# Optimization experiments

Measured on AMD Instinct MI355X. Metric: run time of the kernel, lower is better.

## Reference

```python
import jax, jax.numpy as jnp
import numpy as np

DIM = 128; MOTION = 128; HEADS = 8; WS = 8; B2 = 4; H = 192; W = 192; HID = 512

def _ln(x, w, b, eps=1e-5):
    m = x.mean(-1, keepdims=True)
    v = ((x - m) ** 2).mean(-1, keepdims=True)
    return (x - m) / jnp.sqrt(v + eps) * w + b

def _win_part(x, ws):
    B, Hh, Ww, C = x.shape
    x = x.reshape(B, Hh // ws, ws, Ww // ws, ws, C).transpose(0, 1, 3, 2, 4, 5)
    return x.reshape(-1, ws * ws, C)

def _win_rev(win, ws, Hh, Ww):
    nwB, N, C = win.shape
    B = nwB // ((Hh // ws) * (Ww // ws))
    x = win.reshape(B, Hh // ws, Ww // ws, ws, ws, C).transpose(0, 1, 3, 2, 4, 5)
    return x.reshape(B, Hh, Ww, C)

def setup_inputs() -> dict:
    key = jax.random.key(0)
    ks = jax.random.split(key, 12)
    def lin(k, o, i):
        return jax.random.normal(k, (o, i), jnp.float32) * 0.02
    return {
        "x": jax.random.normal(ks[0], (B2, H * W, DIM), jnp.float32),
        "cor": jax.random.uniform(ks[1], (B2, H * W, 2), dtype=jnp.float32),
        "q_w": lin(ks[2], DIM, DIM),
        "kv_w": lin(ks[3], 2 * DIM, DIM),
        "cor_w": lin(ks[4], MOTION, 2),
        "proj_w": lin(ks[5], DIM, DIM), "proj_b": jnp.zeros((DIM,), jnp.float32),
        "mproj_w": lin(ks[6], MOTION, MOTION), "mproj_b": jnp.zeros((MOTION,), jnp.float32),
        "norm1_w": jnp.ones((DIM,), jnp.float32), "norm1_b": jnp.zeros((DIM,), jnp.float32),
        "norm2_w": jnp.ones((DIM,), jnp.float32), "norm2_b": jnp.zeros((DIM,), jnp.float32),
        "fc1_w": lin(ks[7], HID, DIM), "fc1_b": jnp.zeros((HID,), jnp.float32),
        "dw_w": jax.random.normal(ks[8], (HID, 1, 3, 3), jnp.float32) * 0.1,
        "dw_b": jnp.zeros((HID,), jnp.float32),
        "fc2_w": lin(ks[9], DIM, HID), "fc2_b": jnp.zeros((DIM,), jnp.float32),
    }

def _attn(x1, x2, cor, q_w, kv_w, cor_w, proj_w, proj_b, mproj_w, mproj_b):
    # x1,x2: (nwB, N, C) windowed query / cross-frame key-value; cor: (nwB, N, 2)
    B, N, C = x1.shape
    hd = C // HEADS
    mh = MOTION // HEADS
    scale = hd ** -0.5
    q = (x1 @ q_w.T).reshape(B, N, HEADS, hd).transpose(0, 2, 1, 3)
    kv = (x2 @ kv_w.T).reshape(B, N, 2, HEADS, hd).transpose(2, 0, 3, 1, 4)
    k, v = kv[0], kv[1]
    ce = cor @ cor_w.T                                   # (B, N, MOTION)
    ceh = ce.reshape(B, N, HEADS, mh).transpose(0, 2, 1, 3)
    attn = jax.nn.softmax(jnp.einsum('bhnd,bhmd->bhnm', q, k) * scale, axis=-1)
    xo = jnp.einsum('bhnm,bhmd->bhnd', attn, v).transpose(0, 2, 1, 3).reshape(B, N, C)
    crev = jnp.einsum('bhnm,bhmd->bhnd', attn, ceh).transpose(0, 2, 1, 3).reshape(B, N, MOTION)
    motion = (crev - ce) @ mproj_w.T + mproj_b
    return xo @ proj_w.T + proj_b, motion

def _mlp(x, fc1_w, fc1_b, dw_w, dw_b, fc2_w, fc2_b):
    B, N, _ = x.shape
    h = x @ fc1_w.T + fc1_b                              # (B, N, HID)
    hm = h.transpose(0, 2, 1).reshape(B, HID, H, W)
    hm = jax.lax.conv_general_dilated(hm, dw_w, (1, 1), 'SAME',
                                      feature_group_count=HID,
                                      dimension_numbers=('NCHW', 'OIHW', 'NCHW'))
    hm = hm + dw_b[None, :, None, None]
    h = jax.nn.gelu(hm.reshape(B, HID, N).transpose(0, 2, 1), approximate=False)
    return h @ fc2_w.T + fc2_b

def reference(x, cor, q_w, kv_w, cor_w, proj_w, proj_b, mproj_w, mproj_b,
              norm1_w, norm1_b, norm2_w, norm2_b, fc1_w, fc1_b, dw_w, dw_b, fc2_w, fc2_b):
    shortcut = x
    xn = _ln(x, norm1_w, norm1_b).reshape(B2, H, W, DIM)
    cm = cor.reshape(B2, H, W, 2)
    xw = _win_part(xn, WS)                               # (nwB, 64, DIM)
    cw = _win_part(cm, WS)
    nwB = xw.shape[0]
    xr = jnp.concatenate([xw[nwB // 2:], xw[:nwB // 2]], axis=0)
    xa, xm = _attn(xw, xr, cw, q_w, kv_w, cor_w, proj_w, proj_b, mproj_w, mproj_b)
    xa = _win_rev(xa, WS, H, W).reshape(B2, H * W, DIM)
    xm = _win_rev(xm, WS, H, W).reshape(B2, H * W, MOTION)
    x = shortcut + xa
    x = x + _mlp(_ln(x, norm2_w, norm2_b), fc1_w, fc1_b, dw_w, dw_b, fc2_w, fc2_b)
    return x, xm
```

## Files before the change

kernel.cpp:

```cpp
#include <hip/hip_runtime.h>
#include <hip/hip_bf16.h>
#include <math.h>

#define NB 4
#define IMG 192
#define HW (IMG*IMG)
#define T_TOT (NB*HW)
#define HID 512
#define NWB 2304
#define WPB 576
#define NWS 24

typedef __bf16 bf16;
typedef __bf16 bf8 __attribute__((ext_vector_type(8)));
typedef __bf16 bf4 __attribute__((ext_vector_type(4)));
typedef float f32x4 __attribute__((ext_vector_type(4)));

#define MFMA(a,b,c) __builtin_amdgcn_mfma_f32_16x16x32_bf16(a,b,c,0,0,0)

__device__ __forceinline__ int swz128(int row, int col){ return row*128 + (col ^ ((row&7)<<3)); }

__device__ __forceinline__ bf8 zero_bf8(){
  bf8 z = { (bf16)0.f,(bf16)0.f,(bf16)0.f,(bf16)0.f,(bf16)0.f,(bf16)0.f,(bf16)0.f,(bf16)0.f };
  return z;
}
__device__ __forceinline__ f32x4 zero_f4(){ f32x4 z = {0.f,0.f,0.f,0.f}; return z; }

__global__ void k_cvt(const float* __restrict__ s, bf16* __restrict__ d, int n, float scale){
  int i = blockIdx.x*256 + threadIdx.x;
  if (i < n) d[i] = (bf16)(s[i]*scale);
}

__global__ void k_a2(const float* __restrict__ mproj_w, const float* __restrict__ cor_w,
                     bf16* __restrict__ a2w){
  int idx = blockIdx.x*256 + threadIdx.x;
  if (idx >= 4096) return;
  int o = idx >> 5, k = idx & 31;
  float acc = 0.f;
  if (k < 16){
    int h = k >> 1, c = k & 1;
    #pragma unroll
    for (int i=0;i<16;i++)
      acc += mproj_w[o*128 + h*16 + i] * cor_w[(h*16+i)*2 + c];
  }
  a2w[o*32 + k] = (bf16)acc;
}

__global__ __launch_bounds__(256) void k_ln1(
    const float* __restrict__ x, const float* __restrict__ cor,
    const float* __restrict__ n1w, const float* __restrict__ n1b,
    bf16* __restrict__ xn, bf16* __restrict__ cwb)
{
  int tid = threadIdx.x, wm = tid>>6, l = tid&63;
  int lr = l & 15, tg = l >> 4;
  int t = blockIdx.x*16 + wm*4 + tg;

  const float* xp = x + (size_t)t*128 + lr*8;
  float4 a = *(const float4*)xp;
  float4 b4 = *(const float4*)(xp+4);
  float s  = a.x+a.y+a.z+a.w + b4.x+b4.y+b4.z+b4.w;
  float sq = a.x*a.x+a.y*a.y+a.z*a.z+a.w*a.w + b4.x*b4.x+b4.y*b4.y+b4.z*b4.z+b4.w*b4.w;
  #pragma unroll
  for (int m=1;m<16;m<<=1){ s += __shfl_xor(s,m,16); sq += __shfl_xor(sq,m,16); }
  float mean = s * (1.0f/128.0f);
  float var  = sq * (1.0f/128.0f) - mean*mean;
  float rstd = rsqrtf(var + 1e-5f);

  float4 nw0 = *(const float4*)(n1w + lr*8), nw1 = *(const float4*)(n1w + lr*8 + 4);
  float4 nb0 = *(const float4*)(n1b + lr*8), nb1 = *(const float4*)(n1b + lr*8 + 4);

  bf8 o;
  o[0] = (bf16)((a.x -mean)*rstd*nw0.x + nb0.x);
  o[1] = (bf16)((a.y -mean)*rstd*nw0.y + nb0.y);
  o[2] = (bf16)((a.z -mean)*rstd*nw0.z + nb0.z);
  o[3] = (bf16)((a.w -mean)*rstd*nw0.w + nb0.w);
  o[4] = (bf16)((b4.x-mean)*rstd*nw1.x + nb1.x);
  o[5] = (bf16)((b4.y-mean)*rstd*nw1.y + nb1.y);
  o[6] = (bf16)((b4.z-mean)*rstd*nw1.z + nb1.z);
  o[7] = (bf16)((b4.w-mean)*rstd*nw1.w + nb1.w);

  int b = t / HW, r = t % HW;
  int yy = r / IMG, xx = r % IMG;
  int win = b*WPB + (yy>>3)*NWS + (xx>>3);
  int n = ((yy&7)<<3) + (xx&7);
  *(bf8*)(xn + (size_t)win*8192 + n*128 + lr*8) = o;

  if (lr < 2) cwb[(size_t)win*128 + n*2 + lr] = (bf16)cor[(size_t)t*2 + lr];
}

__global__ __launch_bounds__(256) void k_attn(
    const bf16* __restrict__ xn, const bf16* __restrict__ cw,
    const bf16* __restrict__ wq, const bf16* __restrict__ wkv,
    const bf16* __restrict__ wpj, const bf16* __restrict__ a2w,
    const float* __restrict__ proj_b, const float* __restrict__ mproj_b,
    const float* __restrict__ x_in, float* __restrict__ x1, float* __restrict__ out_m)
{
  __shared__ __align__(16) bf16 s_s [64*128];
  __shared__ __align__(16) bf16 s_k [64*128];
  __shared__ __align__(16) bf16 s_vT[128*64];
  __shared__ __align__(16) bf16 s_P [2][64*64];
  __shared__ __align__(16) bf16 s_cT[16*64];
  __shared__ __align__(16) bf16 s_D [64*32];

  int tid = threadIdx.x, wm = tid>>6, l = tid&63;
  int lr = l & 15, lg = l >> 4;
  int win = blockIdx.x;
  int partner = (win + NWB/2) % NWB;
  const bf16* xw_g = xn + (size_t)win*8192;
  const bf16* xr_g = xn + (size_t)partner*8192;

  bf8 xrv[4], xwv[4];
  #pragma unroll
  for (int tci=0;tci<4;tci++){
    int chunk = tid + tci*256;
    int row = chunk>>4, c0 = (chunk&15)*8;
    xrv[tci] = *(const bf8*)(xr_g + row*128 + c0);
    xwv[tci] = *(const bf8*)(xw_g + row*128 + c0);
  }
  bf16 cwv = (bf16)0.f;
  if (tid < 128) cwv = cw[(size_t)win*128 + tid];

  *(unsigned long long*)&s_cT[tid*4] = 0ull;
  *(unsigned long long*)&s_D[tid*8]   = 0ull;
  *(unsigned long long*)&s_D[tid*8+4] = 0ull;
  #pragma unroll
  for (int tci=0;tci<4;tci++){
    int chunk = tid + tci*256;
    int row = chunk>>4, c0 = (chunk&15)*8;
    *(bf8*)&s_s[swz128(row,c0)] = xrv[tci];
  }
  __syncthreads();

  if (tid < 128){
    int c = tid & 1, m = tid >> 1;
    s_cT[c*64 + (m ^ (c<<3))] = cwv;
  } else if (tid < 192){
    int m = tid - 128;
    s_cT[2*64 + (m ^ 16)] = (bf16)1.0f;
  }
  {
    bf8 af[4];
    #pragma unroll
    for (int ks=0;ks<4;ks++) af[ks] = *(const bf8*)&s_s[swz128(wm*16+lr, ks*32 + lg*8)];
    #pragma unroll
    for (int nt=0;nt<8;nt++){
      f32x4 acc = zero_f4();
      #pragma unroll
      for (int ks=0;ks<4;ks++){
        bf8 bfr = *(const bf8*)(wkv + (nt*16+lr)*128 + ks*32 + lg*8);
        acc = MFMA(af[ks], bfr, acc);
      }
      #pragma unroll
      for (int j=0;j<4;j++){
        int row = wm*16 + lg*4 + j;
        s_k[swz128(row, nt*16+lr)] = (bf16)acc[j];
      }
    }
    #pragma unroll
    for (int nt=0;nt<8;nt++){
      f32x4 acc = zero_f4();
      #pragma unroll
      for (int ks=0;ks<4;ks++){
        bf8 bfr = *(const bf8*)(wkv + (128 + nt*16+lr)*128 + ks*32 + lg*8);
        acc = MFMA(af[ks], bfr, acc);
      }
      #pragma unroll
      for (int j=0;j<4;j++){
        int tok = wm*16 + lg*4 + j;
        int chc = nt*16 + lr;
        s_vT[chc*64 + (tok ^ ((chc&7)<<3))] = (bf16)acc[j];
      }
    }
  }
  __syncthreads();

  #pragma unroll
  for (int tci=0;tci<4;tci++){
    int chunk = tid + tci*256;
    int row = chunk>>4, c0 = (chunk&15)*8;
    *(bf8*)&s_s[swz128(row,c0)] = xwv[tci];
  }
  __syncthreads();

  {
    bf8 af[4];
    #pragma unroll
    for (int ks=0;ks<4;ks++) af[ks] = *(const bf8*)&s_s[swz128(wm*16+lr, ks*32 + lg*8)];
    #pragma unroll
    for (int nt=0;nt<8;nt++){
      f32x4 acc = zero_f4();
      #pragma unroll
      for (int ks=0;ks<4;ks++){
        bf8 bfr = *(const bf8*)(wq + (nt*16+lr)*128 + ks*32 + lg*8);
        acc = MFMA(af[ks], bfr, acc);
      }
      #pragma unroll
      for (int j=0;j<4;j++){
        int row = wm*16 + lg*4 + j;
        s_s[swz128(row, nt*16+lr)] = (bf16)acc[j];
      }
    }
  }

  float mycw[4] = {0.f,0.f,0.f,0.f};
  if (lr < 2){
    #pragma unroll
    for (int j=0;j<4;j++){
      int row = wm*16 + lg*4 + j;
      mycw[j] = (float)s_cT[lr*64 + (row ^ (lr<<3))];
    }
  }

  #pragma unroll
  for (int h=0;h<8;h++){
    bf8 aS = zero_bf8();
    if (l < 32) aS = *(const bf8*)&s_s[swz128(wm*16+lr, h*16 + lg*8)];
    f32x4 accS[4];
    #pragma unroll
    for (int nt=0;nt<4;nt++){
      bf8 bSv = zero_bf8();
      if (l < 32) bSv = *(const bf8*)&s_k[swz128(nt*16+lr, h*16 + lg*8)];
      accS[nt] = MFMA(aS, bSv, zero_f4());
    }
    bf16* Pb = &s_P[h&1][0];
    #pragma unroll
    for (int nt=0;nt<4;nt++){
      #pragma unroll
      for (int j=0;j<4;j++){
        int row = wm*16 + lg*4 + j;
        Pb[row*64 + ((nt*16+lr) ^ ((row&7)<<3))] = (bf16)__expf(accS[nt][j]);
      }
    }
    f32x4 accO = zero_f4(), accPC = zero_f4();
    #pragma unroll
    for (int ks=0;ks<2;ks++){
      int rowA = wm*16 + lr;
      bf8 aP = *(const bf8*)&Pb[rowA*64 + ((ks*32 + lg*8) ^ ((rowA&7)<<3))];
      int chc = h*16 + lr;
      bf8 bV = *(const bf8*)&s_vT[chc*64 + ((ks*32 + lg*8) ^ ((chc&7)<<3))];
      accO = MFMA(aP, bV, accO);
      bf8 bC = *(const bf8*)&s_cT[lr*64 + ((ks*32 + lg*8) ^ ((lr&7)<<3))];
      accPC = MFMA(aP, bC, accPC);
    }
    #pragma unroll
    for (int j=0;j<4;j++){
      int row = wm*16 + lg*4 + j;
      float rs = __shfl(accPC[j], (l & 48) + 2, 64);
      float inv = __builtin_amdgcn_rcpf(rs);
      s_s[swz128(row, h*16+lr)] = (bf16)(accO[j]*inv);
      if (lr < 2)
        s_D[row*32 + ((2*h+lr) ^ ((row&3)<<3))] = (bf16)(accPC[j]*inv - mycw[j]);
    }
  }

  int b  = win / WPB, wi = win % WPB;
  int wy = wi / NWS,  wx = wi % NWS;
  {
    bf8 af[4];
    #pragma unroll
    for (int ks=0;ks<4;ks++) af[ks] = *(const bf8*)&s_s[swz128(wm*16+lr, ks*32 + lg*8)];
    #pragma unroll
    for (int nt=0;nt<8;nt++){
      f32x4 acc = zero_f4();
      #pragma unroll
      for (int ks=0;ks<4;ks++){
        bf8 bfr = *(const bf8*)(wpj + (nt*16+lr)*128 + ks*32 + lg*8);
        acc = MFMA(af[ks], bfr, acc);
      }
      int col = nt*16 + lr;
      float pb = proj_b[col];
      #pragma unroll
      for (int j=0;j<4;j++){
        int tok = wm*16 + lg*4 + j;
        int yy = wy*8 + (tok>>3), xx = wx*8 + (tok&7);
        size_t addr = ((size_t)b*HW + yy*IMG + xx)*128 + col;
        x1[addr] = acc[j] + pb + x_in[addr];
      }
    }
  }
  {
    int rowA = wm*16 + lr;
    bf8 afD = *(const bf8*)&s_D[rowA*32 + ((lg*8) ^ ((rowA&3)<<3))];
    #pragma unroll
    for (int nt=0;nt<8;nt++){
      bf8 bfr = *(const bf8*)(a2w + (nt*16+lr)*32 + lg*8);
      f32x4 acc = MFMA(afD, bfr, zero_f4());
      int col = nt*16 + lr;
      float pb = mproj_b[col];
      #pragma unroll
      for (int j=0;j<4;j++){
        int tok = wm*16 + lg*4 + j;
        int yy = wy*8 + (tok>>3), xx = wx*8 + (tok&7);
        size_t addr = ((size_t)b*HW + yy*IMG + xx)*128 + col;
        out_m[addr] = acc[j] + pb;
      }
    }
  }
}

__global__ __launch_bounds__(256) void k_fc1(
    const float* __restrict__ x1, const float* __restrict__ n2w, const float* __restrict__ n2b,
    const bf16* __restrict__ wf1, const float* __restrict__ fc1b, bf16* __restrict__ h)
{
  __shared__ __align__(16) bf16 s_a[64*128];
  int tid = threadIdx.x, wm = tid>>6, l = tid&63;
  int lr = l & 15, lg = l >> 4;
  size_t t0 = (size_t)blockIdx.x * 64;

  float4 nw0 = *(const float4*)(n2w + lr*8), nw1 = *(const float4*)(n2w + lr*8 + 4);
  float4 nb0 = *(const float4*)(n2b + lr*8), nb1 = *(const float4*)(n2b + lr*8 + 4);

  #pragma unroll
  for (int rr=0; rr<4; rr++){
    int row = wm*16 + rr*4 + lg;
    const float* xp = x1 + (t0+row)*128 + lr*8;
    float4 a = *(const float4*)xp;
    float4 b4 = *(const float4*)(xp+4);
    float s  = a.x+a.y+a.z+a.w + b4.x+b4.y+b4.z+b4.w;
    float sq = a.x*a.x+a.y*a.y+a.z*a.z+a.w*a.w + b4.x*b4.x+b4.y*b4.y+b4.z*b4.z+b4.w*b4.w;
    #pragma unroll
    for (int m=1;m<16;m<<=1){ s += __shfl_xor(s,m,16); sq += __shfl_xor(sq,m,16); }
    float mean = s*(1.f/128.f), var = sq*(1.f/128.f) - mean*mean;
    float rstd = rsqrtf(var + 1e-5f);
    bf8 o;
    o[0] = (bf16)((a.x -mean)*rstd*nw0.x + nb0.x);
    o[1] = (bf16)((a.y -mean)*rstd*nw0.y + nb0.y);
    o[2] = (bf16)((a.z -mean)*rstd*nw0.z + nb0.z);
    o[3] = (bf16)((a.w -mean)*rstd*nw0.w + nb0.w);
    o[4] = (bf16)((b4.x-mean)*rstd*nw1.x + nb1.x);
    o[5] = (bf16)((b4.y-mean)*rstd*nw1.y + nb1.y);
    o[6] = (bf16)((b4.z-mean)*rstd*nw1.z + nb1.z);
    o[7] = (bf16)((b4.w-mean)*rstd*nw1.w + nb1.w);
    *(bf8*)&s_a[swz128(row, lr*8)] = o;
  }
  __syncthreads();

  bf8 af[4];
  #pragma unroll
  for (int ks=0;ks<4;ks++) af[ks] = *(const bf8*)&s_a[swz128(wm*16+lr, ks*32 + lg*8)];
  for (int ntb=0; ntb<4; ntb++){
    f32x4 acc[8];
    #pragma unroll
    for (int q8=0;q8<8;q8++){
      acc[q8] = zero_f4();
      #pragma unroll
      for (int ks=0;ks<4;ks++){
        int ocol = ntb*128 + q8*16 + lr;
        bf8 bfr = *(const bf8*)(wf1 + (size_t)ocol*128 + ks*32 + lg*8);
        acc[q8] = MFMA(af[ks], bfr, acc[q8]);
      }
    }
    #pragma unroll
    for (int q8=0;q8<8;q8++){
      int col = ntb*128 + q8*16 + lr;
      float bb = fc1b[col];
      #pragma unroll
      for (int j=0;j<4;j++){
        int tl = wm*16 + lg*4 + j;
        h[(t0+tl)*512 + col] = (bf16)(acc[q8][j] + bb);
      }
    }
  }
}

__global__ __launch_bounds__(256) void k_mlp2(
    const bf16* __restrict__ h, const float* __restrict__ dww, const float* __restrict__ dwb,
    const bf16* __restrict__ wf2, const float* __restrict__ fc2b,
    const float* __restrict__ x1, float* __restrict__ outx)
{
  __shared__ __align__(16) bf16 s_hh[100*128];
  __shared__ __align__(16) bf16 s_a [64*128];
  int tid = threadIdx.x, wm = tid>>6, l = tid&63;
  int lr = l & 15, lg = l >> 4;
  int tile = blockIdx.x, b = blockIdx.y;
  int ty = tile / 24, tx = tile % 24;
  int cq = (tid & 31) * 4;
  int tg = tid >> 5;

  f32x4 acc[8];
  #pragma unroll
  for (int q=0;q<8;q++) acc[q] = zero_f4();

  for (int kc=0;kc<4;kc++){
    for (int it=0; it<7; it++){
      int idx = it*256 + tid;
      if (idx < 1600){
        int pos = idx>>4, c0 = (idx&15)*8;
        int hy = pos/10, hx = pos%10;
        int yy = ty*8 + hy - 1, xx = tx*8 + hx - 1;
        bf8 v;
        if (yy>=0 && yy<IMG && xx>=0 && xx<IMG)
          v = *(const bf8*)(h + ((size_t)b*HW + yy*IMG + xx)*512 + kc*128 + c0);
        else v = zero_bf8();
        *(bf8*)&s_hh[pos*128 + c0] = v;
      }
    }
    __syncthreads();
    {
      int chg0 = kc*128 + cq;
      float wflat[36];
      #pragma unroll
      for (int q=0;q<9;q++){
        float4 t4 = *(const float4*)(dww + chg0*9 + q*4);
        wflat[q*4+0]=t4.x; wflat[q*4+1]=t4.y; wflat[q*4+2]=t4.z; wflat[q*4+3]=t4.w;
      }
      float4 bias4 = *(const float4*)(dwb + chg0);
      float bb[4] = {bias4.x, bias4.y, bias4.z, bias4.w};
      #pragma unroll
      for (int i=0;i<8;i++){
        int tok = tg*8 + i;
        int iy = tok>>3, ix = tok&7;
        float s4[4] = {bb[0],bb[1],bb[2],bb[3]};
        #pragma unroll
        for (int dy=0;dy<3;dy++){
          #pragma unroll
          for (int dx=0;dx<3;dx++){
            bf4 pv = *(const bf4*)&s_hh[((iy+dy)*10 + ix+dx)*128 + cq];
            #pragma unroll
            for (int c=0;c<4;c++) s4[c] += (float)pv[c] * wflat[c*9 + dy*3+dx];
          }
        }
        bf4 g4;
        #pragma unroll
        for (int c=0;c<4;c++){
          float g = 0.5f*s4[c]*(1.0f + erff(s4[c]*0.70710678118654752f));
          g4[c] = (bf16)g;
        }
        *(bf4*)&s_a[swz128(tok,cq)] = g4;
      }
    }
    __syncthreads();
    {
      bf8 af[4];
      #pragma unroll
      for (int ks=0;ks<4;ks++) af[ks] = *(const bf8*)&s_a[swz128(wm*16+lr, ks*32 + lg*8)];
      #pragma unroll
      for (int q=0;q<8;q++){
        #pragma unroll
        for (int ks=0;ks<4;ks++){
          bf8 bfr = *(const bf8*)(wf2 + (size_t)(q*16+lr)*512 + kc*128 + ks*32 + lg*8);
          acc[q] = MFMA(af[ks], bfr, acc[q]);
        }
      }
    }
    __syncthreads();
  }
  #pragma unroll
  for (int q=0;q<8;q++){
    int col = q*16 + lr;
    float bb = fc2b[col];
    #pragma unroll
    for (int j=0;j<4;j++){
      int tok = wm*16 + lg*4 + j;
      int yy = ty*8 + (tok>>3), xx = tx*8 + (tok&7);
      size_t addr = ((size_t)b*HW + yy*IMG + xx)*128 + col;
      outx[addr] = acc[q][j] + bb + x1[addr];
    }
  }
}

extern "C" void kernel_launch(void* const* d_in, const int* in_sizes, int n_in,
                              void* d_out, int out_size, void* d_ws, size_t ws_size,
                              hipStream_t stream)
{
  const float* x      = (const float*)d_in[0];
  const float* cor    = (const float*)d_in[1];
  const float* q_w    = (const float*)d_in[2];
  const float* kv_w   = (const float*)d_in[3];
  const float* cor_w  = (const float*)d_in[4];
  const float* proj_w = (const float*)d_in[5];
  const float* proj_b = (const float*)d_in[6];
  const float* mproj_w= (const float*)d_in[7];
  const float* mproj_b= (const float*)d_in[8];
  const float* n1w    = (const float*)d_in[9];
  const float* n1b    = (const float*)d_in[10];
  const float* n2w    = (const float*)d_in[11];
  const float* n2b    = (const float*)d_in[12];
  const float* fc1w   = (const float*)d_in[13];
  const float* fc1b   = (const float*)d_in[14];
  const float* dww    = (const float*)d_in[15];
  const float* dwb    = (const float*)d_in[16];
  const float* fc2w   = (const float*)d_in[17];
  const float* fc2b   = (const float*)d_in[18];
  float* out = (float*)d_out;

  char* ws = (char*)d_ws;
  bf16* wq   = (bf16*)(ws + 0);
  bf16* wkv  = (bf16*)(ws + 32768);
  bf16* wpj  = (bf16*)(ws + 98304);
  bf16* a2w  = (bf16*)(ws + 131072);
  bf16* wf1  = (bf16*)(ws + 139264);
  bf16* wf2  = (bf16*)(ws + 270336);
  bf16* xn   = (bf16*)(ws + 401408);
  bf16* cwb  = (bf16*)(ws + 38150144);
  float* x1  = (float*)(ws + 38739968);
  bf16* hbuf = (bf16*)(ws + 114237440);

  k_cvt<<<64,  256, 0, stream>>>(q_w,   wq,  16384, 0.25f);
  k_cvt<<<128, 256, 0, stream>>>(kv_w,  wkv, 32768, 1.0f);
  k_cvt<<<64,  256, 0, stream>>>(proj_w,wpj, 16384, 1.0f);
  k_cvt<<<256, 256, 0, stream>>>(fc1w,  wf1, 65536, 1.0f);
  k_cvt<<<256, 256, 0, stream>>>(fc2w,  wf2, 65536, 1.0f);
  k_a2 <<<16,  256, 0, stream>>>(mproj_w, cor_w, a2w);

  k_ln1 <<<T_TOT/16, 256, 0, stream>>>(x, cor, n1w, n1b, xn, cwb);
  k_attn<<<NWB,      256, 0, stream>>>(xn, cwb, wq, wkv, wpj, a2w, proj_b, mproj_b,
                                       x, x1, out + (size_t)T_TOT*128);
  k_fc1 <<<T_TOT/64, 256, 0, stream>>>(x1, n2w, n2b, wf1, fc1b, hbuf);
  k_mlp2<<<dim3(576,4), 256, 0, stream>>>(hbuf, dww, dwb, wf2, fc2b, x1, out);
}
```

Baseline: 559.8 us.

## Restructure k_mlp2 depthwise conv to reuse halo LDS and tanh-approx GELU

Drops the separate s_a LDS buffer: the GELU output is written back into the halo tile's interior (XOR-swizzled) and read from there for the MFMA, and the halo row is padded to 136 to reduce bank conflicts. The depthwise conv loop is reordered so each tap weight is loaded once and applied across eight tokens. Exact erf GELU is replaced by a tanh-style sigmoid approximation using exp and rcp. The launch bound now requests 5 blocks per CU to raise occupancy, at the cost of register pressure and a small accuracy change from the approximate GELU.

```diff
diff --git a/kernel.cpp b/kernel.cpp
--- a/kernel.cpp
+++ b/kernel.cpp
@@ -363,13 +363,12 @@
   }
 }
 
-__global__ __launch_bounds__(256) void k_mlp2(
+__global__ __launch_bounds__(256, 5) void k_mlp2(
     const bf16* __restrict__ h, const float* __restrict__ dww, const float* __restrict__ dwb,
     const bf16* __restrict__ wf2, const float* __restrict__ fc2b,
     const float* __restrict__ x1, float* __restrict__ outx)
 {
-  __shared__ __align__(16) bf16 s_hh[100*128];
-  __shared__ __align__(16) bf16 s_a [64*128];
+  __shared__ __align__(16) bf16 s_hh[100*136];
   int tid = threadIdx.x, wm = tid>>6, l = tid&63;
   int lr = l & 15, lg = l >> 4;
   int tile = blockIdx.x, b = blockIdx.y;
@@ -382,6 +381,7 @@
   for (int q=0;q<8;q++) acc[q] = zero_f4();
 
   for (int kc=0;kc<4;kc++){
+    __syncthreads();
     for (int it=0; it<7; it++){
       int idx = it*256 + tid;
       if (idx < 1600){
@@ -392,48 +392,60 @@
         if (yy>=0 && yy<IMG && xx>=0 && xx<IMG)
           v = *(const bf8*)(h + ((size_t)b*HW + yy*IMG + xx)*512 + kc*128 + c0);
         else v = zero_bf8();
-        *(bf8*)&s_hh[pos*128 + c0] = v;
+        *(bf8*)&s_hh[pos*136 + c0] = v;
       }
     }
     __syncthreads();
-    {
-      int chg0 = kc*128 + cq;
-      float wflat[36];
-      #pragma unroll
-      for (int q=0;q<9;q++){
-        float4 t4 = *(const float4*)(dww + chg0*9 + q*4);
-        wflat[q*4+0]=t4.x; wflat[q*4+1]=t4.y; wflat[q*4+2]=t4.z; wflat[q*4+3]=t4.w;
-      }
-      float4 bias4 = *(const float4*)(dwb + chg0);
-      float bb[4] = {bias4.x, bias4.y, bias4.z, bias4.w};
-      #pragma unroll
-      for (int i=0;i<8;i++){
-        int tok = tg*8 + i;
-        int iy = tok>>3, ix = tok&7;
-        float s4[4] = {bb[0],bb[1],bb[2],bb[3]};
+    int chg0 = kc*128 + cq;
+    float4 bias4 = *(const float4*)(dwb + chg0);
+    float cr[8][4];
+    #pragma unroll
+    for (int i=0;i<8;i++){ cr[i][0]=bias4.x; cr[i][1]=bias4.y; cr[i][2]=bias4.z; cr[i][3]=bias4.w; }
+    #pragma unroll
+    for (int dy=0;dy<3;dy++){
+      #pragma unroll
+      for (int dx=0;dx<3;dx++){
+        int tq = dy*3+dx;
+        float w0 = dww[(chg0+0)*9 + tq];
+        float w1 = dww[(chg0+1)*9 + tq];
+        float w2 = dww[(chg0+2)*9 + tq];
+        float w3 = dww[(chg0+3)*9 + tq];
         #pragma unroll
-        for (int dy=0;dy<3;dy++){
-          #pragma unroll
-          for (int dx=0;dx<3;dx++){
-            bf4 pv = *(const bf4*)&s_hh[((iy+dy)*10 + ix+dx)*128 + cq];
-            #pragma unroll
-            for (int c=0;c<4;c++) s4[c] += (float)pv[c] * wflat[c*9 + dy*3+dx];
-          }
+        for (int i=0;i<8;i++){
+          bf4 pv = *(const bf4*)&s_hh[((tg+dy)*10 + (i+dx))*136 + cq];
+          cr[i][0] += (float)pv[0]*w0;
+          cr[i][1] += (float)pv[1]*w1;
+          cr[i][2] += (float)pv[2]*w2;
+          cr[i][3] += (float)pv[3]*w3;
         }
-        bf4 g4;
-        #pragma unroll
-        for (int c=0;c<4;c++){
-          float g = 0.5f*s4[c]*(1.0f + erff(s4[c]*0.70710678118654752f));
-          g4[c] = (bf16)g;
-        }
-        *(bf4*)&s_a[swz128(tok,cq)] = g4;
+      }
+    }
+    bf4 gout[8];
+    #pragma unroll
+    for (int i=0;i<8;i++){
+      #pragma unroll
+      for (int c=0;c<4;c++){
+        float hv = cr[i][c];
+        float hv2 = hv*hv;
+        float v = hv * fmaf(hv2, -0.0713548353f, -1.5957691216f);
+        float g = hv * __builtin_amdgcn_rcpf(1.0f + __expf(v));
+        gout[i][c] = (bf16)g;
       }
     }
     __syncthreads();
+    #pragma unroll
+    for (int i=0;i<8;i++){
+      int pos = (tg+1)*10 + (i+1);
+      *(bf4*)&s_hh[pos*136 + (cq ^ (i<<3))] = gout[i];
+    }
     {
       bf8 af[4];
       #pragma unroll
-      for (int ks=0;ks<4;ks++) af[ks] = *(const bf8*)&s_a[swz128(wm*16+lr, ks*32 + lg*8)];
+      for (int ks=0;ks<4;ks++){
+        int tok = wm*16 + lr;
+        int pos = ((tok>>3)+1)*10 + (tok&7) + 1;
+        af[ks] = *(const bf8*)&s_hh[pos*136 + ((ks*32 + lg*8) ^ ((lr&7)<<3))];
+      }
       #pragma unroll
       for (int q=0;q<8;q++){
         #pragma unroll
@@ -443,7 +455,6 @@
         }
       }
     }
-    __syncthreads();
   }
   #pragma unroll
   for (int q=0;q<8;q++){
```

After: 780.0 us. 1.39x slower.
